# Kernel tuning notes

Measured on AMD Instinct MI355X. Metric: run time of the kernel, lower is better.

## Reference

```python
import jax, jax.numpy as jnp
import numpy as np

N_NODES = 100000
N_EDGES = 600000
N_GRAPHS = 256
D_IN, D_HID, N_CLS = 256, 128, 10
LEAKY_SLOPE = 0.01  # torch default


def gcn_conv(x, W, b, row, col, edge_weight, num_nodes):
    # PyG gcn_norm with add_self_loops=False:
    # deg[j] = sum of edge_weight into target j; norm = d^-1/2[row] * w * d^-1/2[col]
    deg = jax.ops.segment_sum(edge_weight, col, num_segments=num_nodes)
    dis = jnp.where(deg > 0, jax.lax.rsqrt(jnp.where(deg > 0, deg, 1.0)), 0.0)
    norm = dis[row] * edge_weight * dis[col]
    h = x @ W                                   # [N, H] dense GEMM first (as GCNConv does)
    msg = norm[:, None] * h[row]                # [E, H] gather + scale
    out = jax.ops.segment_sum(msg, col, num_segments=num_nodes)  # scatter-add
    return out + b


def setup_inputs() -> dict:
    key = jax.random.key(0)
    ks = jax.random.split(key, 10)
    x = jax.random.normal(ks[0], (N_NODES, D_IN), dtype=jnp.float32)
    edge_index = jax.random.randint(ks[1], (2, N_EDGES), 0, N_NODES, dtype=jnp.int64)
    edge_weight = jax.random.uniform(ks[2], (N_EDGES,), dtype=jnp.float32)
    batch = jnp.sort(jax.random.randint(ks[3], (N_NODES,), 0, N_GRAPHS, dtype=jnp.int64))
    s1 = 1.0 / np.sqrt(D_IN)
    s2 = 1.0 / np.sqrt(D_HID)
    W1 = jax.random.uniform(ks[4], (D_IN, D_HID), jnp.float32, -s1, s1)
    b1 = jnp.zeros((D_HID,), jnp.float32)
    W2 = jax.random.uniform(ks[5], (D_HID, D_HID), jnp.float32, -s2, s2)
    b2 = jnp.zeros((D_HID,), jnp.float32)
    Wl = jax.random.uniform(ks[6], (D_HID, N_CLS), jnp.float32, -s2, s2)
    bl = jax.random.uniform(ks[7], (N_CLS,), jnp.float32, -s2, s2)
    return {"x": x, "edge_index": edge_index, "edge_weight": edge_weight, "batch": batch,
            "W1": W1, "b1": b1, "W2": W2, "b2": b2, "Wl": Wl, "bl": bl}


def reference(x, edge_index, edge_weight, batch, W1, b1, W2, b2, Wl, bl):
    # Eval-mode forward: dropout is identity (training=False).
    row, col = edge_index[0], edge_index[1]
    h = gcn_conv(x, W1, b1, row, col, edge_weight, N_NODES)
    h = jnp.where(h >= 0, h, LEAKY_SLOPE * h)
    h = gcn_conv(h, W2, b2, row, col, edge_weight, N_NODES)
    h = jnp.where(h >= 0, h, LEAKY_SLOPE * h)
    # global mean pool over graphs
    sums = jax.ops.segment_sum(h, batch, num_segments=N_GRAPHS)          # [G, H]
    cnts = jax.ops.segment_sum(jnp.ones((h.shape[0],), h.dtype), batch, num_segments=N_GRAPHS)
    pooled = sums / jnp.maximum(cnts, 1.0)[:, None]
    logits = pooled @ Wl + bl
    return jax.nn.log_softmax(logits, axis=1)
```

## Files before the change

### kernel.cpp

```cpp
#include <hip/hip_runtime.h>

typedef float f32x4 __attribute__((ext_vector_type(4)));
typedef short bf16x8 __attribute__((ext_vector_type(8)));

#define SLOPE 0.01f
#define BKT 64

__device__ __forceinline__ short f2bf(float f) {
    unsigned int u = __float_as_uint(f);
    unsigned int r = (u + 0x7fffu + ((u >> 16) & 1u)) >> 16;
    return (short)r;
}

__global__ void k_init(const float* __restrict__ W1, const float* __restrict__ W2,
                       short* __restrict__ wf1, short* __restrict__ wf2,
                       int* __restrict__ cnt,
                       float* __restrict__ sums, float* __restrict__ cnts, int N, int G) {
    int t = blockIdx.x * blockDim.x + threadIdx.x;
    if (t < 4096) {
        int ntile = t >> 9;
        int ks = (t >> 6) & 7;
        int lane = t & 63;
        int h = lane >> 4, c = lane & 15;
#pragma unroll
        for (int j = 0; j < 8; j++) {
            int k = ks * 32 + h * 8 + j;
            wf1[t * 8 + j] = f2bf(W1[k * 128 + ntile * 16 + c]);
        }
    } else if (t < 6144) {
        int s = t - 4096;
        int ntile = s >> 8;
        int ks = (s >> 6) & 3;
        int lane = s & 63;
        int h = lane >> 4, c = lane & 15;
#pragma unroll
        for (int j = 0; j < 8; j++) {
            int k = ks * 32 + h * 8 + j;
            wf2[s * 8 + j] = f2bf(W2[k * 128 + ntile * 16 + c]);
        }
    } else {
        long u = t - 6144;
        if (u < N) cnt[u] = 0;
        else {
            long v = u - N;
            if (v < (long)G * 128) sums[v] = 0.f;
            else if (v < (long)G * 128 + G) cnts[v - (long)G * 128] = 0.f;
        }
    }
}

__global__ __launch_bounds__(256, 3) void k_gemm1_hist(
        const float* __restrict__ Av, const short* __restrict__ Wf,
        ushort* __restrict__ out, int M, int gemmBlocks,
        const int* __restrict__ ei, const float* __restrict__ ew,
        int* __restrict__ cnt, uint2* __restrict__ ebuf,
        int E, int histBlocks) {
    __shared__ short lds[4 * 8 * 64 * 8];
    const int tid = threadIdx.x;
    int b = blockIdx.x;
    int nInter = 2 * (gemmBlocks < histBlocks ? gemmBlocks : histBlocks);
    bool isGemm; int idx;
    if (b < nInter) { isGemm = (b & 1) == 0; idx = b >> 1; }
    else {
        int r = b - nInter;
        if (gemmBlocks < histBlocks) { isGemm = false; idx = gemmBlocks + r; }
        else                         { isGemm = true;  idx = histBlocks + r; }
    }

    if (!isGemm) {
        int base = idx * 256 + tid;
        int stride = histBlocks * 256;
        int iv[4]; bool av[4]; int cv[4]; int rv[4]; float wv2[4]; int pv[4];
#pragma unroll
        for (int k = 0; k < 4; k++) { iv[k] = base + k * stride; av[k] = iv[k] < E; }
#pragma unroll
        for (int k = 0; k < 4; k++) if (av[k]) cv[k] = ei[E + iv[k]];
#pragma unroll
        for (int k = 0; k < 4; k++) if (av[k]) { rv[k] = ei[iv[k]]; wv2[k] = ew[iv[k]]; }
#pragma unroll
        for (int k = 0; k < 4; k++) if (av[k]) pv[k] = atomicAdd(&cnt[cv[k]], 1);
#pragma unroll
        for (int k = 0; k < 4; k++)
            if (av[k] && pv[k] < BKT)
                ebuf[(long)cv[k] * BKT + pv[k]] = make_uint2((unsigned)rv[k], __float_as_uint(wv2[k]));
        return;
    }

    const int lane = tid & 63;
    const int wid = tid >> 6;
    const int h = lane >> 4, c = lane & 15;
    const int rowW = idx * 128 + wid * 32;

    bf16x8 afr[2][8];
#pragma unroll
    for (int rg = 0; rg < 2; rg++) {
        int arow = rowW + rg * 16 + c;
        if (arow >= M) arow = M - 1;
        const float* arp = Av + (long)arow * 256 + h * 8;
#pragma unroll
        for (int ks = 0; ks < 8; ks++) {
            float4 a0 = *(const float4*)(arp + ks * 32);
            float4 a1 = *(const float4*)(arp + ks * 32 + 4);
            bf16x8 f;
            f[0] = f2bf(a0.x); f[1] = f2bf(a0.y); f[2] = f2bf(a0.z); f[3] = f2bf(a0.w);
            f[4] = f2bf(a1.x); f[5] = f2bf(a1.y); f[6] = f2bf(a1.z); f[7] = f2bf(a1.w);
            afr[rg][ks] = f;
        }
    }

    const bf16x8* lf8 = (const bf16x8*)lds;
#pragma unroll
    for (int half = 0; half < 2; half++) {
        if (half) __syncthreads();
        {
            const float4* wsrc = (const float4*)Wf + half * 2048;
            float4* wdst = (float4*)lds;
#pragma unroll
            for (int i = 0; i < 8; i++)
                wdst[i * 256 + tid] = wsrc[i * 256 + tid];
        }
        __syncthreads();
#pragma unroll
        for (int ntl = 0; ntl < 4; ntl++) {
            int nt = half * 4 + ntl;
            bf16x8 bfr[8];
#pragma unroll
            for (int ks = 0; ks < 8; ks++)
                bfr[ks] = lf8[(ntl * 8 + ks) * 64 + lane];
            f32x4 acc0 = {0.f, 0.f, 0.f, 0.f}, acc1 = {0.f, 0.f, 0.f, 0.f};
#pragma unroll
            for (int ks = 0; ks < 8; ks++) {
                acc0 = __builtin_amdgcn_mfma_f32_16x16x32_bf16(bfr[ks], afr[0][ks], acc0, 0, 0, 0);
                acc1 = __builtin_amdgcn_mfma_f32_16x16x32_bf16(bfr[ks], afr[1][ks], acc1, 0, 0, 0);
            }
#pragma unroll
            for (int rg = 0; rg < 2; rg++) {
                f32x4 acc = rg ? acc1 : acc0;
                int orow = rowW + rg * 16 + c;
                if (orow < M) {
                    ushort4 pk;
                    pk.x = (ushort)f2bf(acc[0]); pk.y = (ushort)f2bf(acc[1]);
                    pk.z = (ushort)f2bf(acc[2]); pk.w = (ushort)f2bf(acc[3]);
                    *(ushort4*)(out + (long)orow * 128 + nt * 16 + h * 4) = pk;
                }
            }
        }
    }
}

__global__ void k_dn(const int* __restrict__ cnt, uint2* __restrict__ ebuf,
                     float* __restrict__ dis, int N) {
    int gid = blockIdx.x * blockDim.x + threadIdx.x;
    int n = gid >> 3, e = gid & 7;
    if (n >= N) return;
    int m = min(cnt[n], BKT);
    uint2* p = ebuf + (long)n * BKT;
    float wv[8];
    float d = 0.f;
#pragma unroll
    for (int k = 0; k < 8; k++) {
        int i = e + k * 8;
        wv[k] = 0.f;
        if (i < m) { wv[k] = __uint_as_float(p[i].y); d += wv[k]; }
    }
    d += __shfl_xor(d, 1);
    d += __shfl_xor(d, 2);
    d += __shfl_xor(d, 4);
    float di = d > 0.f ? rsqrtf(d) : 0.f;
    if (e == 0) dis[n] = di;
#pragma unroll
    for (int k = 0; k < 8; k++) {
        int i = e + k * 8;
        if (i < m) p[i].y = __float_as_uint(wv[k] * di);
    }
}

__global__ __launch_bounds__(256, 4) void k_gemm2(const ushort* __restrict__ Av,
                                                  const short* __restrict__ Wf,
                                                  ushort* __restrict__ out, int M) {
    __shared__ short lds[4 * 8 * 64 * 8];
    const int tid = threadIdx.x;
    {
        const float4* wsrc = (const float4*)Wf;
        float4* wdst = (float4*)lds;
#pragma unroll
        for (int i = 0; i < 8; i++)
            wdst[i * 256 + tid] = wsrc[i * 256 + tid];
    }
    __syncthreads();

    const int lane = tid & 63;
    const int wid = tid >> 6;
    const int h = lane >> 4, c = lane & 15;
    const int rowW = blockIdx.x * 128 + wid * 32;

    bf16x8 afr[2][4];
#pragma unroll
    for (int rg = 0; rg < 2; rg++) {
        int arow = rowW + rg * 16 + c;
        if (arow >= M) arow = M - 1;
        const ushort* arp = Av + (long)arow * 128 + h * 8;
#pragma unroll
        for (int ks = 0; ks < 4; ks++)
            afr[rg][ks] = *(const bf16x8*)(arp + ks * 32);
    }

    const bf16x8* lf8 = (const bf16x8*)lds;
#pragma unroll
    for (int nt = 0; nt < 8; nt++) {
        bf16x8 bfr[4];
#pragma unroll
        for (int ks = 0; ks < 4; ks++)
            bfr[ks] = lf8[(nt * 4 + ks) * 64 + lane];
        f32x4 acc0 = {0.f, 0.f, 0.f, 0.f}, acc1 = {0.f, 0.f, 0.f, 0.f};
#pragma unroll
        for (int ks = 0; ks < 4; ks++) {
            acc0 = __builtin_amdgcn_mfma_f32_16x16x32_bf16(bfr[ks], afr[0][ks], acc0, 0, 0, 0);
            acc1 = __builtin_amdgcn_mfma_f32_16x16x32_bf16(bfr[ks], afr[1][ks], acc1, 0, 0, 0);
        }
#pragma unroll
        for (int rg = 0; rg < 2; rg++) {
            f32x4 acc = rg ? acc1 : acc0;
            int orow = rowW + rg * 16 + c;
            if (orow < M) {
                ushort4 pk;
                pk.x = (ushort)f2bf(acc[0]); pk.y = (ushort)f2bf(acc[1]);
                pk.z = (ushort)f2bf(acc[2]); pk.w = (ushort)f2bf(acc[3]);
                *(ushort4*)(out + (long)orow * 128 + nt * 16 + h * 4) = pk;
            }
        }
    }
}

template <int OM>
__global__ __launch_bounds__(256) void k_agg(const uint2* __restrict__ ebuf,
                                             const int* __restrict__ cnt, const float* __restrict__ dis,
                                             const unsigned* __restrict__ hbuf,
                                             unsigned* __restrict__ outp, const float* __restrict__ bias, int N) {
    int wv = (blockIdx.x * blockDim.x + threadIdx.x) >> 6;
    int lane = threadIdx.x & 63;
    if (wv >= N) return;
    long s = (long)wv * BKT;
    int m = min(cnt[wv], BKT);
    float ax = 0.f, ay = 0.f;
    for (int base = 0; base < m; base += 16) {
        int rem = m - base;
        int nact = rem < 16 ? rem : 16;
        uint2 p = make_uint2(0u, 0u);
        float dr = 0.f;
        if (lane < nact) { p = ebuf[s + base + lane]; dr = dis[p.x]; }
        float nrmL = dr * __uint_as_float(p.y);
        int px = (int)p.x;
#pragma unroll
        for (int j = 0; j < 8; j++) {
            unsigned rj = (unsigned)__shfl(px, j);
            float nj = __shfl(nrmL, j);
            unsigned hv = hbuf[(long)rj * 64 + lane];
            ax = fmaf(nj, __uint_as_float(hv << 16), ax);
            ay = fmaf(nj, __uint_as_float(hv & 0xffff0000u), ay);
        }
        if (rem > 8) {
#pragma unroll
            for (int j = 8; j < 16; j++) {
                unsigned rj = (unsigned)__shfl(px, j);
                float nj = __shfl(nrmL, j);
                unsigned hv = hbuf[(long)rj * 64 + lane];
                ax = fmaf(nj, __uint_as_float(hv << 16), ax);
                ay = fmaf(nj, __uint_as_float(hv & 0xffff0000u), ay);
            }
        }
    }
    float vx = ax, vy = ay;
    if (OM == 0) {
        float2 bv = ((const float2*)bias)[lane];
        vx += bv.x; vx = vx < 0.f ? SLOPE * vx : vx;
        vy += bv.y; vy = vy < 0.f ? SLOPE * vy : vy;
    }
    unsigned pk = (unsigned)(ushort)f2bf(vx) | ((unsigned)(ushort)f2bf(vy) << 16);
    outp[(long)wv * 64 + lane] = pk;
}

__global__ __launch_bounds__(64) void k_pool(const unsigned* __restrict__ aggb, const float* __restrict__ b2,
                                             const int* __restrict__ batch, float* __restrict__ sums,
                                             float* __restrict__ cnts, int N) {
    int n0 = blockIdx.x * 128;
    if (n0 >= N) return;
    int t = threadIdx.x;
    float2 bv = ((const float2*)b2)[t];
    int end = min(n0 + 128, N);
    int curg = batch[n0];
    float ax = 0.f, ay = 0.f;
    int run = 0;
    for (int n = n0; n < end; n++) {
        int g = batch[n];
        if (g != curg) {
            atomicAdd(&sums[curg * 128 + 2 * t], ax);
            atomicAdd(&sums[curg * 128 + 2 * t + 1], ay);
            if (t == 0) atomicAdd(&cnts[curg], (float)run);
            ax = ay = 0.f; run = 0; curg = g;
        }
        unsigned pk = aggb[(long)n * 64 + t];
        float vx = __uint_as_float(pk << 16) + bv.x;        vx = vx < 0.f ? SLOPE * vx : vx;
        float vy = __uint_as_float(pk & 0xffff0000u) + bv.y; vy = vy < 0.f ? SLOPE * vy : vy;
        ax += vx; ay += vy; run++;
    }
    atomicAdd(&sums[curg * 128 + 2 * t], ax);
    atomicAdd(&sums[curg * 128 + 2 * t + 1], ay);
    if (t == 0) atomicAdd(&cnts[curg], (float)run);
}

__global__ void k_final(const float* __restrict__ sums, const float* __restrict__ cnts,
                        const float* __restrict__ Wl, const float* __restrict__ bl,
                        float* __restrict__ out, int G) {
    int g = blockIdx.x * blockDim.x + threadIdx.x;
    if (g >= G) return;
    float inv = 1.f / fmaxf(cnts[g], 1.f);
    float l[10];
#pragma unroll
    for (int c = 0; c < 10; c++) l[c] = bl[c];
    for (int k = 0; k < 128; k++) {
        float p = sums[g * 128 + k] * inv;
#pragma unroll
        for (int c = 0; c < 10; c++) l[c] += p * Wl[k * 10 + c];
    }
    float m = l[0];
#pragma unroll
    for (int c = 1; c < 10; c++) m = fmaxf(m, l[c]);
    float s = 0.f;
#pragma unroll
    for (int c = 0; c < 10; c++) s += expf(l[c] - m);
    float lse = m + logf(s);
#pragma unroll
    for (int c = 0; c < 10; c++) out[g * 10 + c] = l[c] - lse;
}

extern "C" void kernel_launch(void* const* d_in, const int* in_sizes, int n_in,
                              void* d_out, int out_size, void* d_ws, size_t ws_size,
                              hipStream_t stream) {
    const float* x  = (const float*)d_in[0];
    const int*   ei = (const int*)d_in[1];
    const float* ew = (const float*)d_in[2];
    const int*   batch = (const int*)d_in[3];
    const float* W1 = (const float*)d_in[4];
    const float* b1 = (const float*)d_in[5];
    const float* W2 = (const float*)d_in[6];
    const float* b2 = (const float*)d_in[7];
    const float* Wl = (const float*)d_in[8];
    const float* bl = (const float*)d_in[9];
    float* out = (float*)d_out;

    const int N = in_sizes[0] / 256;
    const int E = in_sizes[2];
    const int G = out_size / 10;

    char* ws = (char*)d_ws;
    float*  dis  = (float*)(ws);
    int*    cnt  = (int*)  (ws + 400384);
    uint2*  ebuf = (uint2*)(ws + 800768);
    ushort* hbuf = (ushort*)(ws + 52000768);
    ushort* abuf = (ushort*)(ws + 77600768);
    short*  wf1  = (short*)(ws + 103200768);
    short*  wf2  = (short*)(ws + 103266304);
    float*  sums = (float*)(ws + 103299072);
    float*  cnts = (float*)(ws + 103430144);

    long initThreads = 6144 + (long)N + (long)G * 128 + G;
    int initBlocks = (int)((initThreads + 255) / 256);
    k_init<<<initBlocks, 256, 0, stream>>>(W1, W2, wf1, wf2, cnt, sums, cnts, N, G);

    const int GB = (N + 127) / 128;
    const int HB = (E + 1023) / 1024;
    k_gemm1_hist<<<GB + HB, 256, 0, stream>>>(x, wf1, hbuf, N, GB,
                                              ei, ew, cnt, ebuf, E, HB);

    k_dn<<<(N * 8 + 255) / 256, 256, 0, stream>>>(cnt, ebuf, dis, N);

    k_agg<0><<<(N + 3) / 4, 256, 0, stream>>>(ebuf, cnt, dis, (const unsigned*)hbuf, (unsigned*)abuf, b1, N);
    k_gemm2<<<(N + 127) / 128, 256, 0, stream>>>(abuf, wf2, hbuf, N);
    k_agg<1><<<(N + 3) / 4, 256, 0, stream>>>(ebuf, cnt, dis, (const unsigned*)hbuf, (unsigned*)abuf, nullptr, N);

    k_pool<<<(N + 127) / 128, 64, 0, stream>>>((const unsigned*)abuf, b2, batch, sums, cnts, N);
    k_final<<<1, 256, 0, stream>>>(sums, cnts, Wl, bl, out, G);
}
```

Baseline: 195.9 us.

## Fuse mean-pool and classifier into one per-graph kernel using binary search

Replaces the atomic-based pooling kernel and the single-block final kernel with one kernel that launches one 64-thread block per graph. Each block binary-searches the sorted batch array for its node range, accumulates the mean directly, computes logits with a wave shuffle reduction, and applies log-softmax. This removes the atomics, the zeroing of the sums/counts buffers, and a kernel launch. The cost is that only G=256 small blocks run, each looping serially over roughly 390 nodes, which may underuse the GPU.

```diff
diff --git a/kernel.cpp b/kernel.cpp
--- a/kernel.cpp
+++ b/kernel.cpp
@@ -14,8 +14,7 @@
 
 __global__ void k_init(const float* __restrict__ W1, const float* __restrict__ W2,
                        short* __restrict__ wf1, short* __restrict__ wf2,
-                       int* __restrict__ cnt,
-                       float* __restrict__ sums, float* __restrict__ cnts, int N, int G) {
+                       int* __restrict__ cnt, int N) {
     int t = blockIdx.x * blockDim.x + threadIdx.x;
     if (t < 4096) {
         int ntile = t >> 9;
@@ -41,11 +40,6 @@
     } else {
         long u = t - 6144;
         if (u < N) cnt[u] = 0;
-        else {
-            long v = u - N;
-            if (v < (long)G * 128) sums[v] = 0.f;
-            else if (v < (long)G * 128 + G) cnts[v - (long)G * 128] = 0.f;
-        }
     }
 }
 
@@ -280,58 +274,52 @@
     outp[(long)wv * 64 + lane] = pk;
 }
 
-__global__ __launch_bounds__(64) void k_pool(const unsigned* __restrict__ aggb, const float* __restrict__ b2,
-                                             const int* __restrict__ batch, float* __restrict__ sums,
-                                             float* __restrict__ cnts, int N) {
-    int n0 = blockIdx.x * 128;
-    if (n0 >= N) return;
+__global__ __launch_bounds__(64) void k_poolfin(
+        const unsigned* __restrict__ aggb, const float* __restrict__ b2,
+        const int* __restrict__ batch,
+        const float* __restrict__ Wl, const float* __restrict__ bl,
+        float* __restrict__ out, int N) {
+    int g = blockIdx.x;
     int t = threadIdx.x;
+    int lo = 0, hi = N;
+    while (lo < hi) { int mid = (lo + hi) >> 1; if (batch[mid] < g) lo = mid + 1; else hi = mid; }
+    int s = lo;
+    hi = N;
+    while (lo < hi) { int mid = (lo + hi) >> 1; if (batch[mid] < g + 1) lo = mid + 1; else hi = mid; }
+    int e = lo;
+
     float2 bv = ((const float2*)b2)[t];
-    int end = min(n0 + 128, N);
-    int curg = batch[n0];
     float ax = 0.f, ay = 0.f;
-    int run = 0;
-    for (int n = n0; n < end; n++) {
-        int g = batch[n];
-        if (g != curg) {
-            atomicAdd(&sums[curg * 128 + 2 * t], ax);
-            atomicAdd(&sums[curg * 128 + 2 * t + 1], ay);
-            if (t == 0) atomicAdd(&cnts[curg], (float)run);
-            ax = ay = 0.f; run = 0; curg = g;
-        }
+    for (int n = s; n < e; n++) {
         unsigned pk = aggb[(long)n * 64 + t];
         float vx = __uint_as_float(pk << 16) + bv.x;        vx = vx < 0.f ? SLOPE * vx : vx;
         float vy = __uint_as_float(pk & 0xffff0000u) + bv.y; vy = vy < 0.f ? SLOPE * vy : vy;
-        ax += vx; ay += vy; run++;
-    }
-    atomicAdd(&sums[curg * 128 + 2 * t], ax);
-    atomicAdd(&sums[curg * 128 + 2 * t + 1], ay);
-    if (t == 0) atomicAdd(&cnts[curg], (float)run);
-}
-
-__global__ void k_final(const float* __restrict__ sums, const float* __restrict__ cnts,
-                        const float* __restrict__ Wl, const float* __restrict__ bl,
-                        float* __restrict__ out, int G) {
-    int g = blockIdx.x * blockDim.x + threadIdx.x;
-    if (g >= G) return;
-    float inv = 1.f / fmaxf(cnts[g], 1.f);
+        ax += vx; ay += vy;
+    }
+    float inv = 1.f / (float)max(e - s, 1);
+    float px = ax * inv, py = ay * inv;
+
     float l[10];
 #pragma unroll
-    for (int c = 0; c < 10; c++) l[c] = bl[c];
-    for (int k = 0; k < 128; k++) {
-        float p = sums[g * 128 + k] * inv;
-#pragma unroll
-        for (int c = 0; c < 10; c++) l[c] += p * Wl[k * 10 + c];
-    }
-    float m = l[0];
-#pragma unroll
-    for (int c = 1; c < 10; c++) m = fmaxf(m, l[c]);
-    float s = 0.f;
-#pragma unroll
-    for (int c = 0; c < 10; c++) s += expf(l[c] - m);
-    float lse = m + logf(s);
-#pragma unroll
-    for (int c = 0; c < 10; c++) out[g * 10 + c] = l[c] - lse;
+    for (int c = 0; c < 10; c++)
+        l[c] = px * Wl[(2 * t) * 10 + c] + py * Wl[(2 * t + 1) * 10 + c];
+#pragma unroll
+    for (int off = 32; off >= 1; off >>= 1)
+#pragma unroll
+        for (int c = 0; c < 10; c++) l[c] += __shfl_down(l[c], off);
+    if (t == 0) {
+#pragma unroll
+        for (int c = 0; c < 10; c++) l[c] += bl[c];
+        float m = l[0];
+#pragma unroll
+        for (int c = 1; c < 10; c++) m = fmaxf(m, l[c]);
+        float sum = 0.f;
+#pragma unroll
+        for (int c = 0; c < 10; c++) sum += expf(l[c] - m);
+        float lse = m + logf(sum);
+#pragma unroll
+        for (int c = 0; c < 10; c++) out[g * 10 + c] = l[c] - lse;
+    }
 }
 
 extern "C" void kernel_launch(void* const* d_in, const int* in_sizes, int n_in,
@@ -361,12 +349,10 @@
     ushort* abuf = (ushort*)(ws + 77600768);
     short*  wf1  = (short*)(ws + 103200768);
     short*  wf2  = (short*)(ws + 103266304);
-    float*  sums = (float*)(ws + 103299072);
-    float*  cnts = (float*)(ws + 103430144);
-
-    long initThreads = 6144 + (long)N + (long)G * 128 + G;
+
+    long initThreads = 6144 + (long)N;
     int initBlocks = (int)((initThreads + 255) / 256);
-    k_init<<<initBlocks, 256, 0, stream>>>(W1, W2, wf1, wf2, cnt, sums, cnts, N, G);
+    k_init<<<initBlocks, 256, 0, stream>>>(W1, W2, wf1, wf2, cnt, N);
 
     const int GB = (N + 127) / 128;
     const int HB = (E + 1023) / 1024;
@@ -379,6 +365,5 @@
     k_gemm2<<<(N + 127) / 128, 256, 0, stream>>>(abuf, wf2, hbuf, N);
     k_agg<1><<<(N + 3) / 4, 256, 0, stream>>>(ebuf, cnt, dis, (const unsigned*)hbuf, (unsigned*)abuf, nullptr, N);
 
-    k_pool<<<(N + 127) / 128, 64, 0, stream>>>((const unsigned*)abuf, b2, batch, sums, cnts, N);
-    k_final<<<1, 256, 0, stream>>>(sums, cnts, Wl, bl, out, G);
-}
+    k_poolfin<<<G, 64, 0, stream>>>((const unsigned*)abuf, b2, batch, Wl, bl, out, N);
+}
```

Result: slower. 266.2 us (+35.9%).
